# Optimization experiments

Measured on AMD Instinct MI355X. Metric: run time of the kernel, lower is better.

The kernel has to match this reference:

```python
import jax, jax.numpy as jnp
import numpy as np

B, T, DM, DH, DD, V, K = 2, 512, 1024, 4096, 4, 32000, 8
THR = 0.25
EPS = 1e-5
IGN = -100


def setup_inputs() -> dict:
    key = jax.random.key(0)
    ks = jax.random.split(key, 12)
    s = 0.02
    return {
        "H": jax.random.normal(ks[0], (B, T, DM), jnp.float32),
        "input_ids": jax.random.randint(ks[1], (B, T), 0, V),
        "attention_mask": jax.random.randint(ks[2], (B, T), 0, 2),
        "labels": jax.random.randint(ks[3], (B, T), 0, V),
        "emb": s * jax.random.normal(ks[4], (V, DM), jnp.float32),
        "depth_emb": s * jax.random.normal(ks[5], (DD, DM), jnp.float32),
        "ln_g": jnp.ones((DM,), jnp.float32),
        "ln_b": jnp.zeros((DM,), jnp.float32),
        "W1": s * jax.random.normal(ks[6], (DM, DH), jnp.float32),
        "b1": jnp.zeros((DH,), jnp.float32),
        "W2": s * jax.random.normal(ks[7], (DH, DM), jnp.float32),
        "b2": jnp.zeros((DM,), jnp.float32),
        "Wq": s * jax.random.normal(ks[8], (DM, V), jnp.float32),
        "bq": jnp.zeros((V,), jnp.float32),
        "Wb": s * jax.random.normal(ks[9], (DM, 1), jnp.float32),
        "bb": jnp.zeros((1,), jnp.float32),
    }


def _forward(H, input_ids, attention_mask, labels, emb, depth_emb, ln_g, ln_b, W1, b1, W2, b2, Wq, bq, Wb, bb):
    mask = attention_mask.astype(bool)  # (B,T)
    E = emb[input_ids]  # (B,T,DM)
    # draft state: broadcast over depth dim
    S = H[:, :, None, :] + E[:, :, None, :] + depth_emb[None, None]  # (B,T,DD,DM)
    mu = S.mean(-1, keepdims=True)
    var = ((S - mu) ** 2).mean(-1, keepdims=True)  # biased var, as torch LayerNorm
    S = (S - mu) * jax.lax.rsqrt(var + EPS) * ln_g + ln_b
    S = jax.nn.gelu(S @ W1 + b1, approximate=False) @ W2 + b2
    q = S @ Wq + bq  # (B,T,DD,V)
    beta = (S @ Wb + bb)[..., 0]  # (B,T,DD)
    q = jnp.where(mask[:, :, None, None], q, 0.0)
    beta = jnp.where(mask[:, :, None], beta, 0.0)
    # future labels for D depths (small fixed loop over DD)
    targets = jnp.full((B, T, DD), IGN, jnp.int32)
    valid = jnp.zeros((B, T, DD), bool)
    for d in range(1, DD + 1):
        v = mask[:, : T - d] & mask[:, d:]
        valid = valid.at[:, : T - d, d - 1].set(v)
        targets = targets.at[:, : T - d, d - 1].set(
            jnp.where(v, labels[:, d:].astype(jnp.int32), IGN))
    # token CE over valid positions (masked mean)
    logp = jax.nn.log_softmax(q, axis=-1)
    safe = jnp.where(valid, targets, 0)
    nll = -jnp.take_along_axis(logp, safe[..., None], axis=-1)[..., 0]
    cnt = valid.sum()
    L_q = jnp.where(cnt > 0, (nll * valid).sum() / jnp.maximum(cnt, 1).astype(q.dtype), jnp.zeros((), q.dtype))
    # BCE-with-logits on beta, averaged over valid source positions
    bce = jnp.logaddexp(0.0, beta) - beta * valid.astype(beta.dtype)
    src = valid.any(-1, keepdims=True)
    denom = jnp.maximum(src.sum(), 1).astype(beta.dtype)
    L_beta = (bce * src).sum() / denom
    return q, beta, L_q + L_beta


def reference(H, input_ids, attention_mask, labels, emb, depth_emb, ln_g, ln_b, W1, b1, W2, b2, Wq, bq, Wb, bb):
    q, beta, loss = _forward(H, input_ids, attention_mask, labels, emb, depth_emb,
                             ln_g, ln_b, W1, b1, W2, b2, Wq, bq, Wb, bb)
    # dynamic_branch_width
    sigma = jax.nn.sigmoid(beta)
    k = jnp.clip(jnp.ceil(sigma * float(K)).astype(jnp.int32), 1, K)
    k = jnp.where(sigma >= THR, k, 0)
    k = jnp.where(attention_mask.astype(bool)[:, :, None], k, 0)
    return q, beta, k, loss
```

## Files before the change

### kernel.cpp

```cpp
#include <hip/hip_runtime.h>
#include <math.h>

#define B_ 2
#define T_ 512
#define DM_ 1024
#define DH_ 4096
#define DD_ 4
#define V_ 32000
#define M_ 4096
#define BT_ 1024
#define NCHUNK_ 250

typedef __attribute__((ext_vector_type(8))) unsigned short ushort8_t;
typedef __attribute__((ext_vector_type(4))) unsigned short ushort4_t;
typedef __attribute__((ext_vector_type(8))) __bf16 bf16x8;
typedef __attribute__((ext_vector_type(4))) float f32x4;

__device__ __forceinline__ unsigned short f2bf(float x) {
  union { float f; unsigned u; } v; v.f = x;
  unsigned r = v.u + 0x7fffu + ((v.u >> 16) & 1u);
  return (unsigned short)(r >> 16);
}
__device__ __forceinline__ float bf2f(unsigned short h) {
  union { unsigned u; float f; } v; v.u = ((unsigned)h) << 16; return v.f;
}

__device__ __forceinline__ void gload16(const void* g, void* l) {
  __builtin_amdgcn_global_load_lds(
      (const __attribute__((address_space(1))) void*)g,
      (__attribute__((address_space(3))) void*)l, 16, 0, 0);
}

__device__ __forceinline__ void stage_tile(const unsigned short* src, int ld,
                                           unsigned short* lds, int wid, int lane) {
  #pragma unroll
  for (int c = 0; c < 2; ++c) {
    const int rbase = c * 64 + wid * 16;
    const unsigned short* g = src + (size_t)(rbase + (lane >> 2)) * ld + (lane & 3) * 8;
    gload16(g, lds + rbase * 32);
  }
}

__device__ __forceinline__ float block_sum256(float v, float* sh) {
  #pragma unroll
  for (int o = 32; o >= 1; o >>= 1) v += __shfl_down(v, o);
  int lane = threadIdx.x & 63, wid = threadIdx.x >> 6;
  if (lane == 0) sh[wid] = v;
  __syncthreads();
  float t = sh[0] + sh[1] + sh[2] + sh[3];
  __syncthreads();
  return t;
}

__global__ __launch_bounds__(256) void transpose_split_kernel(
    const float* __restrict__ in, int R, int C,
    unsigned short* __restrict__ out_hi, unsigned short* __restrict__ out_lo)
{
  __shared__ float tile[32][33];
  int c0 = blockIdx.x * 32, r0 = blockIdx.y * 32;
  int tx = threadIdx.x & 31, ty = threadIdx.x >> 5;
  #pragma unroll
  for (int i = 0; i < 4; ++i)
    tile[ty + i * 8][tx] = in[(size_t)(r0 + ty + i * 8) * C + c0 + tx];
  __syncthreads();
  #pragma unroll
  for (int i = 0; i < 4; ++i) {
    int orow = c0 + ty + i * 8;
    int ocol = r0 + tx;
    float v = tile[tx][ty + i * 8];
    unsigned short h = f2bf(v);
    out_hi[(size_t)orow * R + ocol] = h;
    if (out_lo) out_lo[(size_t)orow * R + ocol] = f2bf(v - bf2f(h));
  }
}

__global__ __launch_bounds__(256) void embed_ln_kernel(
    const float* __restrict__ H, const int* __restrict__ ids,
    const float* __restrict__ emb, const float* __restrict__ demb,
    const float* __restrict__ g, const float* __restrict__ be,
    unsigned short* __restrict__ Xhi, unsigned short* __restrict__ Xlo)
{
  __shared__ float sh[8];
  int m = blockIdx.x, tid = threadIdx.x;
  int bt = m >> 2, d = m & 3;
  int id = ids[bt];
  float4 x  = ((const float4*)(H   + (size_t)bt * DM_))[tid];
  float4 e  = ((const float4*)(emb + (size_t)id * DM_))[tid];
  float4 de = ((const float4*)(demb + (size_t)d * DM_))[tid];
  float v0 = x.x + e.x + de.x, v1 = x.y + e.y + de.y;
  float v2 = x.z + e.z + de.z, v3 = x.w + e.w + de.w;
  float mu = block_sum256((v0 + v1) + (v2 + v3), sh) * (1.0f / DM_);
  float d0 = v0 - mu, d1v = v1 - mu, d2 = v2 - mu, d3 = v3 - mu;
  float var = block_sum256((d0 * d0 + d1v * d1v) + (d2 * d2 + d3 * d3), sh) * (1.0f / DM_);
  float rs = rsqrtf(var + 1e-5f);
  float4 gg  = ((const float4*)g)[tid];
  float4 bb4 = ((const float4*)be)[tid];
  float y0 = d0 * rs * gg.x + bb4.x;
  float y1 = d1v * rs * gg.y + bb4.y;
  float y2 = d2 * rs * gg.z + bb4.z;
  float y3 = d3 * rs * gg.w + bb4.w;
  unsigned short h0 = f2bf(y0), h1 = f2bf(y1), h2 = f2bf(y2), h3 = f2bf(y3);
  ushort4_t hv = {h0, h1, h2, h3};
  ushort4_t lv = {f2bf(y0 - bf2f(h0)), f2bf(y1 - bf2f(h1)), f2bf(y2 - bf2f(h2)), f2bf(y3 - bf2f(h3))};
  size_t base = (size_t)m * DM_ + tid * 4;
  *(ushort4_t*)&Xhi[base] = hv;
  *(ushort4_t*)&Xlo[base] = lv;
}

__global__ __launch_bounds__(64) void w2b_kernel(
    const float* __restrict__ W2, const float* __restrict__ Wb,
    const float* __restrict__ b2, const float* __restrict__ bb,
    float* __restrict__ w2b)
{
  int j = blockIdx.x, lane = threadIdx.x;
  const float* rowp = (j < DH_) ? (W2 + (size_t)j * DM_) : b2;
  const float4* r4 = (const float4*)rowp;
  const float4* w4 = (const float4*)Wb;
  float s = 0.0f;
  for (int i = lane; i < DM_ / 4; i += 64) {
    float4 a = r4[i], w = w4[i];
    s += a.x * w.x + a.y * w.y + a.z * w.z + a.w * w.w;
  }
  #pragma unroll
  for (int o = 32; o >= 1; o >>= 1) s += __shfl_down(s, o);
  if (lane == 0) w2b[j] = (j < DH_) ? s : (s + bb[0]);
}

template<bool SPLIT, bool GELU, bool CEPART, bool BETAPART, bool NTC>
__global__ __launch_bounds__(256) void gemm_kernel(
    const unsigned short* __restrict__ Ahi, const unsigned short* __restrict__ Alo,
    const unsigned short* __restrict__ Bhi, const unsigned short* __restrict__ Blo,
    const float* __restrict__ bias, int Ndim, int Kdim,
    float* __restrict__ Cf, unsigned short* __restrict__ Chi, unsigned short* __restrict__ Clo,
    const int* __restrict__ rowmask,
    const float* __restrict__ w2bv, float* __restrict__ bpart,
    float* __restrict__ pmax, float* __restrict__ psum)
{
  __shared__ __align__(16) unsigned short sAhi[128 * 32];
  __shared__ __align__(16) unsigned short sBhi[128 * 32];
  __shared__ __align__(16) unsigned short sAlo[SPLIT ? 128 * 32 : 8];
  __shared__ __align__(16) unsigned short sBlo[SPLIT ? 128 * 32 : 8];
  __shared__ float red[(CEPART || BETAPART) ? 512 : 8];

  const int m0 = blockIdx.x * 128, n0 = blockIdx.y * 128;
  const int tid = threadIdx.x, lane = tid & 63, wid = tid >> 6;
  const int wr = wid >> 1, wc = wid & 1;
  const int lrow = lane & 15, koff = (lane >> 4) * 8, q4 = lane >> 4;

  const unsigned short* Ab  = Ahi + (size_t)m0 * Kdim;
  const unsigned short* Bb  = Bhi + (size_t)n0 * Kdim;
  const unsigned short* Alb = SPLIT ? (Alo + (size_t)m0 * Kdim) : nullptr;
  const unsigned short* Blb = SPLIT ? (Blo + (size_t)n0 * Kdim) : nullptr;

  f32x4 acc[4][4] = {};

  for (int k0 = 0; k0 < Kdim; k0 += 32) {
    __syncthreads();
    stage_tile(Ab + k0, Kdim, sAhi, wid, lane);
    stage_tile(Bb + k0, Kdim, sBhi, wid, lane);
    if constexpr (SPLIT) {
      stage_tile(Alb + k0, Kdim, sAlo, wid, lane);
      stage_tile(Blb + k0, Kdim, sBlo, wid, lane);
    }
    asm volatile("s_waitcnt vmcnt(0)" ::: "memory");
    __syncthreads();

    bf16x8 ah[4], bh[4], al[4], bl[4];
    #pragma unroll
    for (int i = 0; i < 4; ++i) {
      ah[i] = __builtin_bit_cast(bf16x8, *(const ushort8_t*)&sAhi[(wr * 64 + i * 16 + lrow) * 32 + koff]);
      bh[i] = __builtin_bit_cast(bf16x8, *(const ushort8_t*)&sBhi[(wc * 64 + i * 16 + lrow) * 32 + koff]);
      if constexpr (SPLIT) {
        al[i] = __builtin_bit_cast(bf16x8, *(const ushort8_t*)&sAlo[(wr * 64 + i * 16 + lrow) * 32 + koff]);
        bl[i] = __builtin_bit_cast(bf16x8, *(const ushort8_t*)&sBlo[(wc * 64 + i * 16 + lrow) * 32 + koff]);
      }
    }
    #pragma unroll
    for (int mi = 0; mi < 4; ++mi)
      #pragma unroll
      for (int ni = 0; ni < 4; ++ni) {
        acc[mi][ni] = __builtin_amdgcn_mfma_f32_16x16x32_bf16(ah[mi], bh[ni], acc[mi][ni], 0, 0, 0);
        if constexpr (SPLIT) {
          acc[mi][ni] = __builtin_amdgcn_mfma_f32_16x16x32_bf16(ah[mi], bl[ni], acc[mi][ni], 0, 0, 0);
          acc[mi][ni] = __builtin_amdgcn_mfma_f32_16x16x32_bf16(al[mi], bh[ni], acc[mi][ni], 0, 0, 0);
        }
      }
  }

  #pragma unroll
  for (int mi = 0; mi < 4; ++mi)
    #pragma unroll
    for (int ni = 0; ni < 4; ++ni) {
      const int col = n0 + wc * 64 + ni * 16 + lrow;
      const float bv = bias ? bias[col] : 0.0f;
      #pragma unroll
      for (int r2 = 0; r2 < 4; ++r2) {
        const int gm = m0 + wr * 64 + mi * 16 + q4 * 4 + r2;
        float v = acc[mi][ni][r2] + bv;
        if constexpr (GELU) v = 0.5f * v * (1.0f + erff(v * 0.70710678118654752440f));
        if (rowmask) v *= (rowmask[gm >> 2] ? 1.0f : 0.0f);
        acc[mi][ni][r2] = v;
        const size_t idx = (size_t)gm * Ndim + col;
        if (Cf) {
          if constexpr (NTC) __builtin_nontemporal_store(v, &Cf[idx]);
          else Cf[idx] = v;
        }
        if (Chi) {
          unsigned short h = f2bf(v);
          Chi[idx] = h;
          if (Clo) Clo[idx] = f2bf(v - bf2f(h));
        }
      }
    }

  if constexpr (CEPART) {
    #pragma unroll
    for (int mi = 0; mi < 4; ++mi)
      #pragma unroll
      for (int r2 = 0; r2 < 4; ++r2) {
        float mx = fmaxf(fmaxf(acc[mi][0][r2], acc[mi][1][r2]),
                         fmaxf(acc[mi][2][r2], acc[mi][3][r2]));
        #pragma unroll
        for (int o = 1; o < 16; o <<= 1) mx = fmaxf(mx, __shfl_xor(mx, o));
        float sm = 0.0f;
        #pragma unroll
        for (int ni = 0; ni < 4; ++ni) sm += expf(acc[mi][ni][r2] - mx);
        #pragma unroll
        for (int o = 1; o < 16; o <<= 1) sm += __shfl_xor(sm, o);
        if (lrow == 0) {
          int r64 = mi * 16 + q4 * 4 + r2;
          red[((wr * 64 + r64) * 2 + wc) * 2 + 0] = mx;
          red[((wr * 64 + r64) * 2 + wc) * 2 + 1] = sm;
        }
      }
    __syncthreads();
    if (tid < 128) {
      int wr2 = tid >> 6, r64 = tid & 63;
      float ma = red[((wr2 * 64 + r64) * 2 + 0) * 2 + 0], sa = red[((wr2 * 64 + r64) * 2 + 0) * 2 + 1];
      float mb = red[((wr2 * 64 + r64) * 2 + 1) * 2 + 0], sb = red[((wr2 * 64 + r64) * 2 + 1) * 2 + 1];
      float mg = fmaxf(ma, mb);
      float sg = sa * expf(ma - mg) + sb * expf(mb - mg);
      int grow = m0 + wr2 * 64 + r64;
      pmax[(size_t)grow * 256 + blockIdx.y] = mg;
      psum[(size_t)grow * 256 + blockIdx.y] = sg;
    }
  }

  if constexpr (BETAPART) {
    #pragma unroll
    for (int mi = 0; mi < 4; ++mi)
      #pragma unroll
      for (int r2 = 0; r2 < 4; ++r2) {
        float s = 0.0f;
        #pragma unroll
        for (int ni = 0; ni < 4; ++ni) {
          const int col = n0 + wc * 64 + ni * 16 + lrow;
          s += acc[mi][ni][r2] * w2bv[col];
        }
        #pragma unroll
        for (int o = 1; o < 16; o <<= 1) s += __shfl_xor(s, o);
        if (lrow == 0)
          red[((wr * 64 + mi * 16 + q4 * 4 + r2) * 2 + wc) * 2 + 0] = s;
      }
    __syncthreads();
    if (tid < 128) {
      int wr2 = tid >> 6, r64 = tid & 63;
      float s = red[((wr2 * 64 + r64) * 2 + 0) * 2 + 0] + red[((wr2 * 64 + r64) * 2 + 1) * 2 + 0];
      bpart[(size_t)(m0 + wr2 * 64 + r64) * 32 + blockIdx.y] = s;
    }
  }
}

__global__ __launch_bounds__(64) void beta_k_kernel(
    const float* __restrict__ bpart, const float* __restrict__ w2b,
    const int* __restrict__ mask,
    float* __restrict__ beta_out, float* __restrict__ k_out,
    float* __restrict__ bce, int* __restrict__ validf)
{
  int m = blockIdx.x, lane = threadIdx.x;
  float s = (lane < 32) ? bpart[(size_t)m * 32 + lane] : 0.0f;
  #pragma unroll
  for (int o = 32; o >= 1; o >>= 1) s += __shfl_down(s, o);
  if (lane == 0) {
    int bt = m >> 2, d1 = (m & 3) + 1;
    float beta = s + w2b[DH_];
    int mv = mask[bt];
    float bm = mv ? beta : 0.0f;
    int t = bt % T_;
    int valid = (t + d1 < T_) && mv && mask[bt + d1];
    beta_out[m] = bm;
    float sp = fmaxf(bm, 0.0f) + log1pf(expf(-fabsf(bm)));
    bce[m] = sp - (valid ? bm : 0.0f);
    validf[m] = valid;
    float sig = 1.0f / (1.0f + expf(-bm));
    int kk = (int)ceilf(sig * 8.0f);
    kk = kk < 1 ? 1 : (kk > 8 ? 8 : kk);
    if (!(sig >= 0.25f)) kk = 0;
    if (!mv) kk = 0;
    k_out[m] = (float)kk;
  }
}

__global__ __launch_bounds__(64) void ce_reduce_kernel(
    const float* __restrict__ pmax, const float* __restrict__ psum,
    const float* __restrict__ q, const int* __restrict__ validf,
    const int* __restrict__ labels, float* __restrict__ nll)
{
  int m = blockIdx.x, lane = threadIdx.x;
  if (!validf[m]) { if (lane == 0) nll[m] = 0.0f; return; }
  float ml = -3.4e38f, sl = 0.0f;
  for (int j = lane; j < NCHUNK_; j += 64) {
    float mj = pmax[(size_t)m * 256 + j], sj = psum[(size_t)m * 256 + j];
    float nm = fmaxf(ml, mj);
    sl = sl * expf(ml - nm) + sj * expf(mj - nm);
    ml = nm;
  }
  #pragma unroll
  for (int o = 32; o >= 1; o >>= 1) {
    float mo = __shfl_xor(ml, o), so = __shfl_xor(sl, o);
    float nm = fmaxf(ml, mo);
    sl = sl * expf(ml - nm) + so * expf(mo - nm);
    ml = nm;
  }
  if (lane == 0) {
    int bt = m >> 2, d1 = (m & 3) + 1;
    float qt = q[(size_t)m * V_ + labels[bt + d1]];
    nll[m] = -(qt - ml - logf(sl));
  }
}

__global__ __launch_bounds__(256) void loss_kernel(
    const float* __restrict__ nll, const int* __restrict__ validf,
    const float* __restrict__ bce, float* __restrict__ loss_out)
{
  __shared__ float sh[8];
  int tid = threadIdx.x;
  float snll = 0.0f, fcnt = 0.0f, sbce = 0.0f, fnsrc = 0.0f;
  for (int m = tid; m < M_; m += 256) { snll += nll[m]; fcnt += (float)validf[m]; }
  for (int bt = tid; bt < BT_; bt += 256) {
    int base = bt * 4;
    int src = validf[base] | validf[base + 1] | validf[base + 2] | validf[base + 3];
    if (src) { sbce += bce[base] + bce[base + 1] + bce[base + 2] + bce[base + 3]; fnsrc += 1.0f; }
  }
  snll = block_sum256(snll, sh);
  fcnt = block_sum256(fcnt, sh);
  sbce = block_sum256(sbce, sh);
  fnsrc = block_sum256(fnsrc, sh);
  if (tid == 0) {
    float Lq = fcnt > 0.0f ? snll / fcnt : 0.0f;
    float Lb = sbce / fmaxf(fnsrc, 1.0f);
    loss_out[0] = Lq + Lb;
  }
}

extern "C" void kernel_launch(void* const* d_in, const int* in_sizes, int n_in,
                              void* d_out, int out_size, void* d_ws, size_t ws_size,
                              hipStream_t stream) {
  const float* H    = (const float*)d_in[0];
  const int*   ids  = (const int*)d_in[1];
  const int*   mask = (const int*)d_in[2];
  const int*   labels = (const int*)d_in[3];
  const float* emb  = (const float*)d_in[4];
  const float* demb = (const float*)d_in[5];
  const float* ln_g = (const float*)d_in[6];
  const float* ln_b = (const float*)d_in[7];
  const float* W1   = (const float*)d_in[8];
  const float* b1   = (const float*)d_in[9];
  const float* W2   = (const float*)d_in[10];
  const float* b2   = (const float*)d_in[11];
  const float* Wq   = (const float*)d_in[12];
  const float* bq   = (const float*)d_in[13];
  const float* Wb   = (const float*)d_in[14];
  const float* bb   = (const float*)d_in[15];

  char* ws = (char*)d_ws; size_t off = 0;
  auto walloc = [&](size_t bytes) -> void* {
    void* p = ws + off; off = (off + bytes + 255) & ~(size_t)255; return p;
  };
  unsigned short* W1t_hi = (unsigned short*)walloc((size_t)DH_ * DM_ * 2);
  unsigned short* W1t_lo = (unsigned short*)walloc((size_t)DH_ * DM_ * 2);
  unsigned short* W2t_hi = (unsigned short*)walloc((size_t)DM_ * DH_ * 2);
  unsigned short* W2t_lo = (unsigned short*)walloc((size_t)DM_ * DH_ * 2);
  unsigned short* Wqt_hi = (unsigned short*)walloc((size_t)V_ * DM_ * 2);
  unsigned short* Xhi    = (unsigned short*)walloc((size_t)M_ * DM_ * 2);
  unsigned short* Xlo    = (unsigned short*)walloc((size_t)M_ * DM_ * 2);
  unsigned short* S2hi   = (unsigned short*)walloc((size_t)M_ * DM_ * 2);
  float* w2b    = (float*)walloc((DH_ + 1) * 4);
  float* bpart  = (float*)walloc((size_t)M_ * 32 * 4);
  float* pmax   = (float*)walloc((size_t)M_ * 256 * 4);
  float* psum   = (float*)walloc((size_t)M_ * 256 * 4);
  float* nll    = (float*)walloc(M_ * 4);
  float* bcev   = (float*)walloc(M_ * 4);
  int*   validf = (int*)walloc(M_ * 4);

  float* q_out    = (float*)d_out;
  float* beta_out = q_out + (size_t)M_ * V_;
  float* k_out    = beta_out + M_;
  float* loss_out = k_out + M_;
  unsigned short* act_hi = (unsigned short*)d_out;
  unsigned short* act_lo = act_hi + (size_t)M_ * DH_;

  transpose_split_kernel<<<dim3(DH_ / 32, DM_ / 32), 256, 0, stream>>>(W1, DM_, DH_, W1t_hi, W1t_lo);
  transpose_split_kernel<<<dim3(DM_ / 32, DH_ / 32), 256, 0, stream>>>(W2, DH_, DM_, W2t_hi, W2t_lo);
  transpose_split_kernel<<<dim3(V_ / 32, DM_ / 32), 256, 0, stream>>>(Wq, DM_, V_, Wqt_hi, nullptr);
  embed_ln_kernel<<<M_, 256, 0, stream>>>(H, ids, emb, demb, ln_g, ln_b, Xhi, Xlo);
  w2b_kernel<<<DH_ + 1, 64, 0, stream>>>(W2, Wb, b2, bb, w2b);
  gemm_kernel<true, true, false, true, false><<<dim3(M_ / 128, DH_ / 128), 256, 0, stream>>>(
      Xhi, Xlo, W1t_hi, W1t_lo, b1, DH_, DM_, nullptr, act_hi, act_lo, nullptr,
      w2b, bpart, nullptr, nullptr);
  beta_k_kernel<<<M_, 64, 0, stream>>>(bpart, w2b, mask, beta_out, k_out, bcev, validf);
  gemm_kernel<true, false, false, false, false><<<dim3(M_ / 128, DM_ / 128), 256, 0, stream>>>(
      act_hi, act_lo, W2t_hi, W2t_lo, b2, DM_, DH_, nullptr, S2hi, nullptr, nullptr,
      nullptr, nullptr, nullptr, nullptr);
  gemm_kernel<false, false, true, false, true><<<dim3(M_ / 128, V_ / 128), 256, 0, stream>>>(
      S2hi, nullptr, Wqt_hi, nullptr, bq, V_, DM_, q_out, nullptr, nullptr, mask,
      nullptr, nullptr, pmax, psum);
  ce_reduce_kernel<<<M_, 64, 0, stream>>>(pmax, psum, q_out, validf, labels, nll);
  loss_kernel<<<1, 256, 0, stream>>>(nll, validf, bcev, loss_out);
}
```

Before: 1.695 ms.

## Double-buffer and swizzle LDS in templated GEMM, enlarge vocab tiles, drop W2 split

```diff
diff --git a/kernel.cpp b/kernel.cpp
--- a/kernel.cpp
+++ b/kernel.cpp
@@ -9,7 +9,8 @@
 #define V_ 32000
 #define M_ 4096
 #define BT_ 1024
-#define NCHUNK_ 250
+#define NCHUNK3_ 125
+#define PCH_ 128
 
 typedef __attribute__((ext_vector_type(8))) unsigned short ushort8_t;
 typedef __attribute__((ext_vector_type(4))) unsigned short ushort4_t;
@@ -31,14 +32,22 @@
       (__attribute__((address_space(3))) void*)l, 16, 0, 0);
 }
 
-__device__ __forceinline__ void stage_tile(const unsigned short* src, int ld,
-                                           unsigned short* lds, int wid, int lane) {
-  #pragma unroll
-  for (int c = 0; c < 2; ++c) {
-    const int rbase = c * 64 + wid * 16;
-    const unsigned short* g = src + (size_t)(rbase + (lane >> 2)) * ld + (lane & 3) * 8;
-    gload16(g, lds + rbase * 32);
-  }
+template<int ROWS, int NWAVE>
+__device__ __forceinline__ void stage_swz(const unsigned short* __restrict__ src, int ld,
+                                          unsigned short* lds, int wid, int lane) {
+  constexpr int NLOAD = ROWS / (16 * NWAVE);
+  const int rl = lane >> 2;
+  const int slot = (lane & 3) ^ ((lane >> 3) & 3);
+  #pragma unroll
+  for (int i = 0; i < NLOAD; ++i) {
+    const int rbase = (i * NWAVE + wid) * 16;
+    gload16(src + (size_t)(rbase + rl) * ld + slot * 8, lds + rbase * 32);
+  }
+}
+
+__device__ __forceinline__ bf16x8 ldfrag(const unsigned short* t, int r, int s) {
+  return __builtin_bit_cast(bf16x8,
+      *(const ushort8_t*)&t[r * 32 + ((s ^ ((r >> 1) & 3)) * 8)]);
 }
 
 __device__ __forceinline__ float block_sum256(float v, float* sh) {
@@ -126,8 +135,9 @@
   if (lane == 0) w2b[j] = (j < DH_) ? s : (s + bb[0]);
 }
 
-template<bool SPLIT, bool GELU, bool CEPART, bool BETAPART, bool NTC>
-__global__ __launch_bounds__(256) void gemm_kernel(
+template<int BM, int BN, int NWAVE, int WN,
+         bool SPLIT, bool GELU, bool CEPART, bool BETAPART, bool NTC>
+__global__ __launch_bounds__(NWAVE * 64, 2) void gemm2p_kernel(
     const unsigned short* __restrict__ Ahi, const unsigned short* __restrict__ Alo,
     const unsigned short* __restrict__ Bhi, const unsigned short* __restrict__ Blo,
     const float* __restrict__ bias, int Ndim, int Kdim,
@@ -136,66 +146,84 @@
     const float* __restrict__ w2bv, float* __restrict__ bpart,
     float* __restrict__ pmax, float* __restrict__ psum)
 {
-  __shared__ __align__(16) unsigned short sAhi[128 * 32];
-  __shared__ __align__(16) unsigned short sBhi[128 * 32];
-  __shared__ __align__(16) unsigned short sAlo[SPLIT ? 128 * 32 : 8];
-  __shared__ __align__(16) unsigned short sBlo[SPLIT ? 128 * 32 : 8];
-  __shared__ float red[(CEPART || BETAPART) ? 512 : 8];
-
-  const int m0 = blockIdx.x * 128, n0 = blockIdx.y * 128;
+  constexpr int WM = NWAVE / WN;
+  constexpr int MI = (BM / WM) / 16;
+  constexpr int NI = (BN / WN) / 16;
+  constexpr int AW = BM * 32;
+  constexpr int BW = BN * 32;
+  constexpr int BUFW = (SPLIT ? 2 : 1) * (AW + BW);
+  __shared__ __align__(16) unsigned short smem[2 * BUFW];
+
+  const int m0 = blockIdx.x * BM, n0 = blockIdx.y * BN;
   const int tid = threadIdx.x, lane = tid & 63, wid = tid >> 6;
-  const int wr = wid >> 1, wc = wid & 1;
-  const int lrow = lane & 15, koff = (lane >> 4) * 8, q4 = lane >> 4;
+  const int wr = wid / WN, wc = wid % WN;
+  const int lrow = lane & 15, q4 = lane >> 4;
+  const int wrb = wr * (BM / WM), wcb = wc * (BN / WN);
 
   const unsigned short* Ab  = Ahi + (size_t)m0 * Kdim;
   const unsigned short* Bb  = Bhi + (size_t)n0 * Kdim;
   const unsigned short* Alb = SPLIT ? (Alo + (size_t)m0 * Kdim) : nullptr;
   const unsigned short* Blb = SPLIT ? (Blo + (size_t)n0 * Kdim) : nullptr;
 
-  f32x4 acc[4][4] = {};
-
-  for (int k0 = 0; k0 < Kdim; k0 += 32) {
-    __syncthreads();
-    stage_tile(Ab + k0, Kdim, sAhi, wid, lane);
-    stage_tile(Bb + k0, Kdim, sBhi, wid, lane);
+  f32x4 acc[MI][NI] = {};
+  const int NT = Kdim / 32;
+
+  auto stageAll = [&](int buf, int kt) {
+    unsigned short* base = smem + buf * BUFW;
+    const int ko = kt * 32;
+    stage_swz<BM, NWAVE>(Ab + ko, Kdim, base, wid, lane);
+    stage_swz<BN, NWAVE>(Bb + ko, Kdim, base + AW, wid, lane);
     if constexpr (SPLIT) {
-      stage_tile(Alb + k0, Kdim, sAlo, wid, lane);
-      stage_tile(Blb + k0, Kdim, sBlo, wid, lane);
+      stage_swz<BM, NWAVE>(Alb + ko, Kdim, base + AW + BW, wid, lane);
+      stage_swz<BN, NWAVE>(Blb + ko, Kdim, base + 2 * AW + BW, wid, lane);
+    }
+  };
+
+  stageAll(0, 0);
+  asm volatile("s_waitcnt vmcnt(0)" ::: "memory");
+  __syncthreads();
+
+  int cur = 0;
+  for (int kt = 0; kt < NT; ++kt) {
+    if (kt + 1 < NT) stageAll(cur ^ 1, kt + 1);
+    __builtin_amdgcn_sched_barrier(0);
+    const unsigned short* sA = smem + cur * BUFW;
+    const unsigned short* sB = sA + AW;
+    bf16x8 bh[NI], bl[NI];
+    #pragma unroll
+    for (int ni = 0; ni < NI; ++ni) {
+      bh[ni] = ldfrag(sB, wcb + ni * 16 + lrow, q4);
+      if constexpr (SPLIT) bl[ni] = ldfrag(sB + AW + BW, wcb + ni * 16 + lrow, q4);
+    }
+    #pragma unroll
+    for (int mi = 0; mi < MI; ++mi) {
+      const int r = wrb + mi * 16 + lrow;
+      bf16x8 ah = ldfrag(sA, r, q4);
+      bf16x8 al;
+      if constexpr (SPLIT) al = ldfrag(sA + AW + BW, r, q4);
+      #pragma unroll
+      for (int ni = 0; ni < NI; ++ni) {
+        acc[mi][ni] = __builtin_amdgcn_mfma_f32_16x16x32_bf16(ah, bh[ni], acc[mi][ni], 0, 0, 0);
+        if constexpr (SPLIT) {
+          acc[mi][ni] = __builtin_amdgcn_mfma_f32_16x16x32_bf16(ah, bl[ni], acc[mi][ni], 0, 0, 0);
+          acc[mi][ni] = __builtin_amdgcn_mfma_f32_16x16x32_bf16(al, bh[ni], acc[mi][ni], 0, 0, 0);
+        }
+      }
     }
     asm volatile("s_waitcnt vmcnt(0)" ::: "memory");
     __syncthreads();
-
-    bf16x8 ah[4], bh[4], al[4], bl[4];
+    cur ^= 1;
+  }
+
+  #pragma unroll
+  for (int mi = 0; mi < MI; ++mi)
     #pragma unroll
-    for (int i = 0; i < 4; ++i) {
-      ah[i] = __builtin_bit_cast(bf16x8, *(const ushort8_t*)&sAhi[(wr * 64 + i * 16 + lrow) * 32 + koff]);
-      bh[i] = __builtin_bit_cast(bf16x8, *(const ushort8_t*)&sBhi[(wc * 64 + i * 16 + lrow) * 32 + koff]);
-      if constexpr (SPLIT) {
-        al[i] = __builtin_bit_cast(bf16x8, *(const ushort8_t*)&sAlo[(wr * 64 + i * 16 + lrow) * 32 + koff]);
-        bl[i] = __builtin_bit_cast(bf16x8, *(const ushort8_t*)&sBlo[(wc * 64 + i * 16 + lrow) * 32 + koff]);
-      }
-    }
-    #pragma unroll
-    for (int mi = 0; mi < 4; ++mi)
-      #pragma unroll
-      for (int ni = 0; ni < 4; ++ni) {
-        acc[mi][ni] = __builtin_amdgcn_mfma_f32_16x16x32_bf16(ah[mi], bh[ni], acc[mi][ni], 0, 0, 0);
-        if constexpr (SPLIT) {
-          acc[mi][ni] = __builtin_amdgcn_mfma_f32_16x16x32_bf16(ah[mi], bl[ni], acc[mi][ni], 0, 0, 0);
-          acc[mi][ni] = __builtin_amdgcn_mfma_f32_16x16x32_bf16(al[mi], bh[ni], acc[mi][ni], 0, 0, 0);
-        }
-      }
-  }
-
-  #pragma unroll
-  for (int mi = 0; mi < 4; ++mi)
-    #pragma unroll
-    for (int ni = 0; ni < 4; ++ni) {
-      const int col = n0 + wc * 64 + ni * 16 + lrow;
+    for (int ni = 0; ni < NI; ++ni) {
+      const int col = n0 + wcb + ni * 16 + lrow;
       const float bv = bias ? bias[col] : 0.0f;
       #pragma unroll
       for (int r2 = 0; r2 < 4; ++r2) {
-        const int gm = m0 + wr * 64 + mi * 16 + q4 * 4 + r2;
+        const int gm = m0 + wrb + mi * 16 + q4 * 4 + r2;
         float v = acc[mi][ni][r2] + bv;
         if constexpr (GELU) v = 0.5f * v * (1.0f + erff(v * 0.70710678118654752440f));
         if (rowmask) v *= (rowmask[gm >> 2] ? 1.0f : 0.0f);
@@ -213,60 +241,64 @@
       }
     }
 
+  float* red = (float*)smem;
+
   if constexpr (CEPART) {
     #pragma unroll
-    for (int mi = 0; mi < 4; ++mi)
+    for (int mi = 0; mi < MI; ++mi)
       #pragma unroll
       for (int r2 = 0; r2 < 4; ++r2) {
-        float mx = fmaxf(fmaxf(acc[mi][0][r2], acc[mi][1][r2]),
-                         fmaxf(acc[mi][2][r2], acc[mi][3][r2]));
+        float mx = -3.4e38f;
+        #pragma unroll
+        for (int ni = 0; ni < NI; ++ni) mx = fmaxf(mx, acc[mi][ni][r2]);
         #pragma unroll
         for (int o = 1; o < 16; o <<= 1) mx = fmaxf(mx, __shfl_xor(mx, o));
         float sm = 0.0f;
         #pragma unroll
-        for (int ni = 0; ni < 4; ++ni) sm += expf(acc[mi][ni][r2] - mx);
+        for (int ni = 0; ni < NI; ++ni) sm += expf(acc[mi][ni][r2] - mx);
         #pragma unroll
         for (int o = 1; o < 16; o <<= 1) sm += __shfl_xor(sm, o);
         if (lrow == 0) {
-          int r64 = mi * 16 + q4 * 4 + r2;
-          red[((wr * 64 + r64) * 2 + wc) * 2 + 0] = mx;
-          red[((wr * 64 + r64) * 2 + wc) * 2 + 1] = sm;
+          const int rowL = wrb + mi * 16 + q4 * 4 + r2;
+          red[(rowL * WN + wc) * 2 + 0] = mx;
+          red[(rowL * WN + wc) * 2 + 1] = sm;
         }
       }
     __syncthreads();
-    if (tid < 128) {
-      int wr2 = tid >> 6, r64 = tid & 63;
-      float ma = red[((wr2 * 64 + r64) * 2 + 0) * 2 + 0], sa = red[((wr2 * 64 + r64) * 2 + 0) * 2 + 1];
-      float mb = red[((wr2 * 64 + r64) * 2 + 1) * 2 + 0], sb = red[((wr2 * 64 + r64) * 2 + 1) * 2 + 1];
-      float mg = fmaxf(ma, mb);
-      float sg = sa * expf(ma - mg) + sb * expf(mb - mg);
-      int grow = m0 + wr2 * 64 + r64;
-      pmax[(size_t)grow * 256 + blockIdx.y] = mg;
-      psum[(size_t)grow * 256 + blockIdx.y] = sg;
+    for (int r = tid; r < BM; r += NWAVE * 64) {
+      float mg = -3.4e38f, sg = 0.0f;
+      #pragma unroll
+      for (int w = 0; w < WN; ++w) {
+        float mw = red[(r * WN + w) * 2 + 0], sw = red[(r * WN + w) * 2 + 1];
+        float nm = fmaxf(mg, mw);
+        sg = sg * expf(mg - nm) + sw * expf(mw - nm);
+        mg = nm;
+      }
+      pmax[(size_t)(m0 + r) * PCH_ + blockIdx.y] = mg;
+      psum[(size_t)(m0 + r) * PCH_ + blockIdx.y] = sg;
     }
   }
 
   if constexpr (BETAPART) {
     #pragma unroll
-    for (int mi = 0; mi < 4; ++mi)
+    for (int mi = 0; mi < MI; ++mi)
       #pragma unroll
       for (int r2 = 0; r2 < 4; ++r2) {
         float s = 0.0f;
         #pragma unroll
-        for (int ni = 0; ni < 4; ++ni) {
-          const int col = n0 + wc * 64 + ni * 16 + lrow;
-          s += acc[mi][ni][r2] * w2bv[col];
-        }
+        for (int ni = 0; ni < NI; ++ni)
+          s += acc[mi][ni][r2] * w2bv[n0 + wcb + ni * 16 + lrow];
         #pragma unroll
         for (int o = 1; o < 16; o <<= 1) s += __shfl_xor(s, o);
         if (lrow == 0)
-          red[((wr * 64 + mi * 16 + q4 * 4 + r2) * 2 + wc) * 2 + 0] = s;
+          red[(wrb + mi * 16 + q4 * 4 + r2) * WN + wc] = s;
       }
     __syncthreads();
-    if (tid < 128) {
-      int wr2 = tid >> 6, r64 = tid & 63;
-      float s = red[((wr2 * 64 + r64) * 2 + 0) * 2 + 0] + red[((wr2 * 64 + r64) * 2 + 1) * 2 + 0];
-      bpart[(size_t)(m0 + wr2 * 64 + r64) * 32 + blockIdx.y] = s;
+    for (int r = tid; r < BM; r += NWAVE * 64) {
+      float s = 0.0f;
+      #pragma unroll
+      for (int w = 0; w < WN; ++w) s += red[r * WN + w];
+      bpart[(size_t)(m0 + r) * 32 + blockIdx.y] = s;
     }
   }
 }
@@ -309,8 +341,8 @@
   int m = blockIdx.x, lane = threadIdx.x;
   if (!validf[m]) { if (lane == 0) nll[m] = 0.0f; return; }
   float ml = -3.4e38f, sl = 0.0f;
-  for (int j = lane; j < NCHUNK_; j += 64) {
-    float mj = pmax[(size_t)m * 256 + j], sj = psum[(size_t)m * 256 + j];
+  for (int j = lane; j < NCHUNK3_; j += 64) {
+    float mj = pmax[(size_t)m * PCH_ + j], sj = psum[(size_t)m * PCH_ + j];
     float nm = fmaxf(ml, mj);
     sl = sl * expf(ml - nm) + sj * expf(mj - nm);
     ml = nm;
@@ -380,15 +412,14 @@
   unsigned short* W1t_hi = (unsigned short*)walloc((size_t)DH_ * DM_ * 2);
   unsigned short* W1t_lo = (unsigned short*)walloc((size_t)DH_ * DM_ * 2);
   unsigned short* W2t_hi = (unsigned short*)walloc((size_t)DM_ * DH_ * 2);
-  unsigned short* W2t_lo = (unsigned short*)walloc((size_t)DM_ * DH_ * 2);
   unsigned short* Wqt_hi = (unsigned short*)walloc((size_t)V_ * DM_ * 2);
   unsigned short* Xhi    = (unsigned short*)walloc((size_t)M_ * DM_ * 2);
   unsigned short* Xlo    = (unsigned short*)walloc((size_t)M_ * DM_ * 2);
   unsigned short* S2hi   = (unsigned short*)walloc((size_t)M_ * DM_ * 2);
   float* w2b    = (float*)walloc((DH_ + 1) * 4);
   float* bpart  = (float*)walloc((size_t)M_ * 32 * 4);
-  float* pmax   = (float*)walloc((size_t)M_ * 256 * 4);
-  float* psum   = (float*)walloc((size_t)M_ * 256 * 4);
+  float* pmax   = (float*)walloc((size_t)M_ * PCH_ * 4);
+  float* psum   = (float*)walloc((size_t)M_ * PCH_ * 4);
   float* nll    = (float*)walloc(M_ * 4);
   float* bcev   = (float*)walloc(M_ * 4);
   int*   validf = (int*)walloc(M_ * 4);
@@ -401,18 +432,21 @@
   unsigned short* act_lo = act_hi + (size_t)M_ * DH_;
 
   transpose_split_kernel<<<dim3(DH_ / 32, DM_ / 32), 256, 0, stream>>>(W1, DM_, DH_, W1t_hi, W1t_lo);
-  transpose_split_kernel<<<dim3(DM_ / 32, DH_ / 32), 256, 0, stream>>>(W2, DH_, DM_, W2t_hi, W2t_lo);
+  transpose_split_kernel<<<dim3(DM_ / 32, DH_ / 32), 256, 0, stream>>>(W2, DH_, DM_, W2t_hi, nullptr);
   transpose_split_kernel<<<dim3(V_ / 32, DM_ / 32), 256, 0, stream>>>(Wq, DM_, V_, Wqt_hi, nullptr);
   embed_ln_kernel<<<M_, 256, 0, stream>>>(H, ids, emb, demb, ln_g, ln_b, Xhi, Xlo);
   w2b_kernel<<<DH_ + 1, 64, 0, stream>>>(W2, Wb, b2, bb, w2b);
-  gemm_kernel<true, true, false, true, false><<<dim3(M_ / 128, DH_ / 128), 256, 0, stream>>>(
+  gemm2p_kernel<128, 128, 8, 4, true, true, false, true, false>
+      <<<dim3(M_ / 128, DH_ / 128), 512, 0, stream>>>(
       Xhi, Xlo, W1t_hi, W1t_lo, b1, DH_, DM_, nullptr, act_hi, act_lo, nullptr,
       w2b, bpart, nullptr, nullptr);
   beta_k_kernel<<<M_, 64, 0, stream>>>(bpart, w2b, mask, beta_out, k_out, bcev, validf);
-  gemm_kernel<true, false, false, false, false><<<dim3(M_ / 128, DM_ / 128), 256, 0, stream>>>(
-      act_hi, act_lo, W2t_hi, W2t_lo, b2, DM_, DH_, nullptr, S2hi, nullptr, nullptr,
+  gemm2p_kernel<128, 128, 4, 2, false, false, false, false, false>
+      <<<dim3(M_ / 128, DM_ / 128), 256, 0, stream>>>(
+      act_hi, nullptr, W2t_hi, nullptr, b2, DM_, DH_, nullptr, S2hi, nullptr, nullptr,
       nullptr, nullptr, nullptr, nullptr);
-  gemm_kernel<false, false, true, false, true><<<dim3(M_ / 128, V_ / 128), 256, 0, stream>>>(
+  gemm2p_kernel<256, 256, 8, 4, false, false, true, false, true>
+      <<<dim3(M_ / 256, V_ / 256), 512, 0, stream>>>(
       S2hi, nullptr, Wqt_hi, nullptr, bq, V_, DM_, q_out, nullptr, nullptr, mask,
       nullptr, nullptr, pmax, psum);
   ce_reduce_kernel<<<M_, 64, 0, stream>>>(pmax, psum, q_out, validf, labels, nll);
```

Result: faster. 1.497 ms (-11.7%).

## Double-buffer GEMM with swizzled LDS, concatenated split-K, and drop W2 lo precision

Applied to the files above, without the earlier changes.

```diff
diff --git a/kernel.cpp b/kernel.cpp
--- a/kernel.cpp
+++ b/kernel.cpp
@@ -9,7 +9,8 @@
 #define V_ 32000
 #define M_ 4096
 #define BT_ 1024
-#define NCHUNK_ 250
+#define NCHUNK3_ 250
+#define PCH_ 256
 
 typedef __attribute__((ext_vector_type(8))) unsigned short ushort8_t;
 typedef __attribute__((ext_vector_type(4))) unsigned short ushort4_t;
@@ -23,22 +24,6 @@
 }
 __device__ __forceinline__ float bf2f(unsigned short h) {
   union { unsigned u; float f; } v; v.u = ((unsigned)h) << 16; return v.f;
-}
-
-__device__ __forceinline__ void gload16(const void* g, void* l) {
-  __builtin_amdgcn_global_load_lds(
-      (const __attribute__((address_space(1))) void*)g,
-      (__attribute__((address_space(3))) void*)l, 16, 0, 0);
-}
-
-__device__ __forceinline__ void stage_tile(const unsigned short* src, int ld,
-                                           unsigned short* lds, int wid, int lane) {
-  #pragma unroll
-  for (int c = 0; c < 2; ++c) {
-    const int rbase = c * 64 + wid * 16;
-    const unsigned short* g = src + (size_t)(rbase + (lane >> 2)) * ld + (lane & 3) * 8;
-    gload16(g, lds + rbase * 32);
-  }
 }
 
 __device__ __forceinline__ float block_sum256(float v, float* sh) {
@@ -51,6 +36,12 @@
   __syncthreads();
   return t;
 }
+
+__device__ __forceinline__ bf16x8 ldfrag(const unsigned short* t, int r, int s) {
+  return __builtin_bit_cast(bf16x8,
+      *(const ushort8_t*)&t[r * 32 + ((s ^ ((r >> 1) & 3)) * 8)]);
+}
+
 
 __global__ __launch_bounds__(256) void transpose_split_kernel(
     const float* __restrict__ in, int R, int C,
@@ -126,76 +117,94 @@
   if (lane == 0) w2b[j] = (j < DH_) ? s : (s + bb[0]);
 }
 
-template<bool SPLIT, bool GELU, bool CEPART, bool BETAPART, bool NTC>
-__global__ __launch_bounds__(256) void gemm_kernel(
-    const unsigned short* __restrict__ Ahi, const unsigned short* __restrict__ Alo,
-    const unsigned short* __restrict__ Bhi, const unsigned short* __restrict__ Blo,
+template<bool CONCAT3, bool GELU, bool CEPART, bool BETAPART, bool NTC>
+__global__ __launch_bounds__(256) void gemmdb_kernel(
+    const unsigned short* __restrict__ A0, const unsigned short* __restrict__ A1,
+    const unsigned short* __restrict__ A2,
+    const unsigned short* __restrict__ B0, const unsigned short* __restrict__ B1,
+    const unsigned short* __restrict__ B2,
     const float* __restrict__ bias, int Ndim, int Kdim,
     float* __restrict__ Cf, unsigned short* __restrict__ Chi, unsigned short* __restrict__ Clo,
     const int* __restrict__ rowmask,
     const float* __restrict__ w2bv, float* __restrict__ bpart,
     float* __restrict__ pmax, float* __restrict__ psum)
 {
-  __shared__ __align__(16) unsigned short sAhi[128 * 32];
-  __shared__ __align__(16) unsigned short sBhi[128 * 32];
-  __shared__ __align__(16) unsigned short sAlo[SPLIT ? 128 * 32 : 8];
-  __shared__ __align__(16) unsigned short sBlo[SPLIT ? 128 * 32 : 8];
-  __shared__ float red[(CEPART || BETAPART) ? 512 : 8];
-
-  const int m0 = blockIdx.x * 128, n0 = blockIdx.y * 128;
+  __shared__ __align__(16) unsigned short sA[2][128 * 32];
+  __shared__ __align__(16) unsigned short sB[2][128 * 32];
+
+  const int nwg = gridDim.x;
+  const int wg = (blockIdx.x & 7) * (nwg >> 3) + (blockIdx.x >> 3);
+  const int by = wg >> 5, bx = wg & 31;
+  const int m0 = bx * 128, n0 = by * 128;
+
   const int tid = threadIdx.x, lane = tid & 63, wid = tid >> 6;
   const int wr = wid >> 1, wc = wid & 1;
-  const int lrow = lane & 15, koff = (lane >> 4) * 8, q4 = lane >> 4;
-
-  const unsigned short* Ab  = Ahi + (size_t)m0 * Kdim;
-  const unsigned short* Bb  = Bhi + (size_t)n0 * Kdim;
-  const unsigned short* Alb = SPLIT ? (Alo + (size_t)m0 * Kdim) : nullptr;
-  const unsigned short* Blb = SPLIT ? (Blo + (size_t)n0 * Kdim) : nullptr;
+  const int lrow = lane & 15, q4 = lane >> 4;
+  const int wrb = wr * 64, wcb = wc * 64;
+
+  const int NT = Kdim >> 5;
+
+  const int r0v = tid >> 2, s0v = tid & 3;
+  const int wA0 = r0v * 32 + ((s0v ^ ((r0v >> 1) & 3)) * 8);
+
+  ushort8_t ra0, ra1, rb0, rb1;
+  auto loadreg = [&](int kt) {
+    const unsigned short* pa; const unsigned short* pb; int ldk, kc;
+    if constexpr (CONCAT3) {
+      pa = (kt < 32) ? A0 : ((kt < 64) ? A1 : A2);
+      pb = (kt < 32) ? B0 : ((kt < 64) ? B1 : B2);
+      ldk = 1024; kc = (kt & 31) * 32;
+    } else {
+      pa = A0; pb = B0; ldk = Kdim; kc = kt * 32;
+    }
+    const unsigned short* ga = pa + (size_t)(m0 + r0v) * ldk + kc + s0v * 8;
+    const unsigned short* gb = pb + (size_t)(n0 + r0v) * ldk + kc + s0v * 8;
+    ra0 = *(const ushort8_t*)ga;  ra1 = *(const ushort8_t*)(ga + (size_t)64 * ldk);
+    rb0 = *(const ushort8_t*)gb;  rb1 = *(const ushort8_t*)(gb + (size_t)64 * ldk);
+  };
+  auto writelds = [&](int b) {
+    *(ushort8_t*)&sA[b][wA0]        = ra0;
+    *(ushort8_t*)&sA[b][wA0 + 2048] = ra1;
+    *(ushort8_t*)&sB[b][wA0]        = rb0;
+    *(ushort8_t*)&sB[b][wA0 + 2048] = rb1;
+  };
 
   f32x4 acc[4][4] = {};
 
-  for (int k0 = 0; k0 < Kdim; k0 += 32) {
-    __syncthreads();
-    stage_tile(Ab + k0, Kdim, sAhi, wid, lane);
-    stage_tile(Bb + k0, Kdim, sBhi, wid, lane);
-    if constexpr (SPLIT) {
-      stage_tile(Alb + k0, Kdim, sAlo, wid, lane);
-      stage_tile(Blb + k0, Kdim, sBlo, wid, lane);
-    }
-    asm volatile("s_waitcnt vmcnt(0)" ::: "memory");
-    __syncthreads();
-
-    bf16x8 ah[4], bh[4], al[4], bl[4];
-    #pragma unroll
-    for (int i = 0; i < 4; ++i) {
-      ah[i] = __builtin_bit_cast(bf16x8, *(const ushort8_t*)&sAhi[(wr * 64 + i * 16 + lrow) * 32 + koff]);
-      bh[i] = __builtin_bit_cast(bf16x8, *(const ushort8_t*)&sBhi[(wc * 64 + i * 16 + lrow) * 32 + koff]);
-      if constexpr (SPLIT) {
-        al[i] = __builtin_bit_cast(bf16x8, *(const ushort8_t*)&sAlo[(wr * 64 + i * 16 + lrow) * 32 + koff]);
-        bl[i] = __builtin_bit_cast(bf16x8, *(const ushort8_t*)&sBlo[(wc * 64 + i * 16 + lrow) * 32 + koff]);
-      }
-    }
+  loadreg(0);
+  writelds(0);
+  if (NT > 1) loadreg(1);
+  __syncthreads();
+
+  for (int kt = 0; kt < NT; ++kt) {
+    const int cur = kt & 1;
+    bf16x8 bh[4], ah[4];
+    #pragma unroll
+    for (int ni = 0; ni < 4; ++ni) bh[ni] = ldfrag(sB[cur], wcb + ni * 16 + lrow, q4);
+    #pragma unroll
+    for (int mi = 0; mi < 4; ++mi) ah[mi] = ldfrag(sA[cur], wrb + mi * 16 + lrow, q4);
+    if (kt + 1 < NT) writelds(cur ^ 1);
+    if (kt + 2 < NT) loadreg(kt + 2);
+    __builtin_amdgcn_sched_barrier(0);
     #pragma unroll
     for (int mi = 0; mi < 4; ++mi)
       #pragma unroll
-      for (int ni = 0; ni < 4; ++ni) {
+      for (int ni = 0; ni < 4; ++ni)
         acc[mi][ni] = __builtin_amdgcn_mfma_f32_16x16x32_bf16(ah[mi], bh[ni], acc[mi][ni], 0, 0, 0);
-        if constexpr (SPLIT) {
-          acc[mi][ni] = __builtin_amdgcn_mfma_f32_16x16x32_bf16(ah[mi], bl[ni], acc[mi][ni], 0, 0, 0);
-          acc[mi][ni] = __builtin_amdgcn_mfma_f32_16x16x32_bf16(al[mi], bh[ni], acc[mi][ni], 0, 0, 0);
-        }
-      }
+    asm volatile("s_waitcnt lgkmcnt(0)" ::: "memory");
+    __builtin_amdgcn_sched_barrier(0);
+    __builtin_amdgcn_s_barrier();
   }
 
   #pragma unroll
   for (int mi = 0; mi < 4; ++mi)
     #pragma unroll
     for (int ni = 0; ni < 4; ++ni) {
-      const int col = n0 + wc * 64 + ni * 16 + lrow;
+      const int col = n0 + wcb + ni * 16 + lrow;
       const float bv = bias ? bias[col] : 0.0f;
       #pragma unroll
       for (int r2 = 0; r2 < 4; ++r2) {
-        const int gm = m0 + wr * 64 + mi * 16 + q4 * 4 + r2;
+        const int gm = m0 + wrb + mi * 16 + q4 * 4 + r2;
         float v = acc[mi][ni][r2] + bv;
         if constexpr (GELU) v = 0.5f * v * (1.0f + erff(v * 0.70710678118654752440f));
         if (rowmask) v *= (rowmask[gm >> 2] ? 1.0f : 0.0f);
@@ -213,13 +222,16 @@
       }
     }
 
+  float* red = (float*)&sA[0][0];
+
   if constexpr (CEPART) {
     #pragma unroll
     for (int mi = 0; mi < 4; ++mi)
       #pragma unroll
       for (int r2 = 0; r2 < 4; ++r2) {
-        float mx = fmaxf(fmaxf(acc[mi][0][r2], acc[mi][1][r2]),
-                         fmaxf(acc[mi][2][r2], acc[mi][3][r2]));
+        float mx = -3.4e38f;
+        #pragma unroll
+        for (int ni = 0; ni < 4; ++ni) mx = fmaxf(mx, acc[mi][ni][r2]);
         #pragma unroll
         for (int o = 1; o < 16; o <<= 1) mx = fmaxf(mx, __shfl_xor(mx, o));
         float sm = 0.0f;
@@ -228,21 +240,19 @@
         #pragma unroll
         for (int o = 1; o < 16; o <<= 1) sm += __shfl_xor(sm, o);
         if (lrow == 0) {
-          int r64 = mi * 16 + q4 * 4 + r2;
-          red[((wr * 64 + r64) * 2 + wc) * 2 + 0] = mx;
-          red[((wr * 64 + r64) * 2 + wc) * 2 + 1] = sm;
+          const int rowL = wrb + mi * 16 + q4 * 4 + r2;
+          red[(rowL * 2 + wc) * 2 + 0] = mx;
+          red[(rowL * 2 + wc) * 2 + 1] = sm;
         }
       }
     __syncthreads();
-    if (tid < 128) {
-      int wr2 = tid >> 6, r64 = tid & 63;
-      float ma = red[((wr2 * 64 + r64) * 2 + 0) * 2 + 0], sa = red[((wr2 * 64 + r64) * 2 + 0) * 2 + 1];
-      float mb = red[((wr2 * 64 + r64) * 2 + 1) * 2 + 0], sb = red[((wr2 * 64 + r64) * 2 + 1) * 2 + 1];
+    for (int r = tid; r < 128; r += 256) {
+      float ma = red[(r * 2 + 0) * 2 + 0], sa = red[(r * 2 + 0) * 2 + 1];
+      float mb = red[(r * 2 + 1) * 2 + 0], sb = red[(r * 2 + 1) * 2 + 1];
       float mg = fmaxf(ma, mb);
       float sg = sa * expf(ma - mg) + sb * expf(mb - mg);
-      int grow = m0 + wr2 * 64 + r64;
-      pmax[(size_t)grow * 256 + blockIdx.y] = mg;
-      psum[(size_t)grow * 256 + blockIdx.y] = sg;
+      pmax[(size_t)(m0 + r) * PCH_ + by] = mg;
+      psum[(size_t)(m0 + r) * PCH_ + by] = sg;
     }
   }
 
@@ -253,23 +263,21 @@
       for (int r2 = 0; r2 < 4; ++r2) {
         float s = 0.0f;
         #pragma unroll
-        for (int ni = 0; ni < 4; ++ni) {
-          const int col = n0 + wc * 64 + ni * 16 + lrow;
-          s += acc[mi][ni][r2] * w2bv[col];
-        }
+        for (int ni = 0; ni < 4; ++ni)
+          s += acc[mi][ni][r2] * w2bv[n0 + wcb + ni * 16 + lrow];
         #pragma unroll
         for (int o = 1; o < 16; o <<= 1) s += __shfl_xor(s, o);
         if (lrow == 0)
-          red[((wr * 64 + mi * 16 + q4 * 4 + r2) * 2 + wc) * 2 + 0] = s;
+          red[(wrb + mi * 16 + q4 * 4 + r2) * 2 + wc] = s;
       }
     __syncthreads();
-    if (tid < 128) {
-      int wr2 = tid >> 6, r64 = tid & 63;
-      float s = red[((wr2 * 64 + r64) * 2 + 0) * 2 + 0] + red[((wr2 * 64 + r64) * 2 + 1) * 2 + 0];
-      bpart[(size_t)(m0 + wr2 * 64 + r64) * 32 + blockIdx.y] = s;
+    for (int r = tid; r < 128; r += 256) {
+      float s = red[r * 2 + 0] + red[r * 2 + 1];
+      bpart[(size_t)(m0 + r) * 32 + by] = s;
     }
   }
 }
+
 
 __global__ __launch_bounds__(64) void beta_k_kernel(
     const float* __restrict__ bpart, const float* __restrict__ w2b,
@@ -309,8 +317,8 @@
   int m = blockIdx.x, lane = threadIdx.x;
   if (!validf[m]) { if (lane == 0) nll[m] = 0.0f; return; }
   float ml = -3.4e38f, sl = 0.0f;
-  for (int j = lane; j < NCHUNK_; j += 64) {
-    float mj = pmax[(size_t)m * 256 + j], sj = psum[(size_t)m * 256 + j];
+  for (int j = lane; j < NCHUNK3_; j += 64) {
+    float mj = pmax[(size_t)m * PCH_ + j], sj = psum[(size_t)m * PCH_ + j];
     float nm = fmaxf(ml, mj);
     sl = sl * expf(ml - nm) + sj * expf(mj - nm);
     ml = nm;
@@ -380,15 +388,14 @@
   unsigned short* W1t_hi = (unsigned short*)walloc((size_t)DH_ * DM_ * 2);
   unsigned short* W1t_lo = (unsigned short*)walloc((size_t)DH_ * DM_ * 2);
   unsigned short* W2t_hi = (unsigned short*)walloc((size_t)DM_ * DH_ * 2);
-  unsigned short* W2t_lo = (unsigned short*)walloc((size_t)DM_ * DH_ * 2);
   unsigned short* Wqt_hi = (unsigned short*)walloc((size_t)V_ * DM_ * 2);
   unsigned short* Xhi    = (unsigned short*)walloc((size_t)M_ * DM_ * 2);
   unsigned short* Xlo    = (unsigned short*)walloc((size_t)M_ * DM_ * 2);
   unsigned short* S2hi   = (unsigned short*)walloc((size_t)M_ * DM_ * 2);
   float* w2b    = (float*)walloc((DH_ + 1) * 4);
   float* bpart  = (float*)walloc((size_t)M_ * 32 * 4);
-  float* pmax   = (float*)walloc((size_t)M_ * 256 * 4);
-  float* psum   = (float*)walloc((size_t)M_ * 256 * 4);
+  float* pmax   = (float*)walloc((size_t)M_ * PCH_ * 4);
+  float* psum   = (float*)walloc((size_t)M_ * PCH_ * 4);
   float* nll    = (float*)walloc(M_ * 4);
   float* bcev   = (float*)walloc(M_ * 4);
   int*   validf = (int*)walloc(M_ * 4);
@@ -401,20 +408,20 @@
   unsigned short* act_lo = act_hi + (size_t)M_ * DH_;
 
   transpose_split_kernel<<<dim3(DH_ / 32, DM_ / 32), 256, 0, stream>>>(W1, DM_, DH_, W1t_hi, W1t_lo);
-  transpose_split_kernel<<<dim3(DM_ / 32, DH_ / 32), 256, 0, stream>>>(W2, DH_, DM_, W2t_hi, W2t_lo);
+  transpose_split_kernel<<<dim3(DM_ / 32, DH_ / 32), 256, 0, stream>>>(W2, DH_, DM_, W2t_hi, nullptr);
   transpose_split_kernel<<<dim3(V_ / 32, DM_ / 32), 256, 0, stream>>>(Wq, DM_, V_, Wqt_hi, nullptr);
   embed_ln_kernel<<<M_, 256, 0, stream>>>(H, ids, emb, demb, ln_g, ln_b, Xhi, Xlo);
   w2b_kernel<<<DH_ + 1, 64, 0, stream>>>(W2, Wb, b2, bb, w2b);
-  gemm_kernel<true, true, false, true, false><<<dim3(M_ / 128, DH_ / 128), 256, 0, stream>>>(
-      Xhi, Xlo, W1t_hi, W1t_lo, b1, DH_, DM_, nullptr, act_hi, act_lo, nullptr,
-      w2b, bpart, nullptr, nullptr);
+  gemmdb_kernel<true, true, false, true, false><<<1024, 256, 0, stream>>>(
+      Xhi, Xhi, Xlo, W1t_hi, W1t_lo, W1t_hi, b1, DH_, 3 * DM_,
+      nullptr, act_hi, act_lo, nullptr, w2b, bpart, nullptr, nullptr);
   beta_k_kernel<<<M_, 64, 0, stream>>>(bpart, w2b, mask, beta_out, k_out, bcev, validf);
-  gemm_kernel<true, false, false, false, false><<<dim3(M_ / 128, DM_ / 128), 256, 0, stream>>>(
-      act_hi, act_lo, W2t_hi, W2t_lo, b2, DM_, DH_, nullptr, S2hi, nullptr, nullptr,
-      nullptr, nullptr, nullptr, nullptr);
-  gemm_kernel<false, false, true, false, true><<<dim3(M_ / 128, V_ / 128), 256, 0, stream>>>(
-      S2hi, nullptr, Wqt_hi, nullptr, bq, V_, DM_, q_out, nullptr, nullptr, mask,
-      nullptr, nullptr, pmax, psum);
+  gemmdb_kernel<false, false, false, false, false><<<256, 256, 0, stream>>>(
+      act_hi, act_hi, act_hi, W2t_hi, W2t_hi, W2t_hi, b2, DM_, DH_,
+      nullptr, S2hi, nullptr, nullptr, nullptr, nullptr, nullptr, nullptr);
+  gemmdb_kernel<false, false, true, false, true><<<8000, 256, 0, stream>>>(
+      S2hi, S2hi, S2hi, Wqt_hi, Wqt_hi, Wqt_hi, bq, V_, DM_,
+      q_out, nullptr, nullptr, mask, nullptr, nullptr, pmax, psum);
   ce_reduce_kernel<<<M_, 64, 0, stream>>>(pmax, psum, q_out, validf, labels, nll);
   loss_kernel<<<1, 256, 0, stream>>>(nll, validf, bcev, loss_out);
 }
```

After: 2.517 ms. 48.5% more time.
